# Kernel optimization log

Hardware: AMD Instinct MI355X
Metric: run time of the kernel (lower is better)

The kernel has to match this reference:

```python
import jax, jax.numpy as jnp
import numpy as np

HIDDEN = 64

def setup_inputs() -> dict:
    key = jax.random.key(0)
    ks = jax.random.split(key, 5)
    N, T, D, H = 4096, 128, 32, HIDDEN
    x = jax.random.normal(ks[0], (N, T, D), dtype=jnp.float32)
    adj_matrix = jax.random.uniform(ks[1], (N, N), dtype=jnp.float32) * (1.0 / N)
    weight_ih = jax.random.normal(ks[2], (D, 4 * H), dtype=jnp.float32) * (1.0 / np.sqrt(D))
    weight_hh = jax.random.normal(ks[3], (H, 4 * H), dtype=jnp.float32) * (1.0 / np.sqrt(H))
    bias = jnp.zeros((4 * H,), dtype=jnp.float32)
    weight_q = jax.random.normal(ks[4], (H, H), dtype=jnp.float32) * (1.0 / np.sqrt(H))
    bias_q = jnp.zeros((H,), dtype=jnp.float32)
    return {"x": x, "adj_matrix": adj_matrix, "weight_ih": weight_ih,
            "weight_hh": weight_hh, "bias": bias, "weight_q": weight_q,
            "bias_q": bias_q}

def reference(x, adj_matrix, weight_ih, weight_hh, bias, weight_q, bias_q):
    # x: [N, T, D]; adj_matrix: [N, N]. Dropout=0 -> identity (eval mode).
    N, T, D = x.shape
    H = weight_hh.shape[0]

    def step(carry, x_t):
        h, c = carry                                   # [N, H], [N, H]
        gates = x_t @ weight_ih + h @ weight_hh + bias  # [N, 4H]
        i_t = jax.nn.sigmoid(gates[:, :H])
        f_t = jax.nn.sigmoid(gates[:, H:2 * H])
        g_t = jnp.tanh(gates[:, 2 * H:3 * H])
        o_t = jax.nn.sigmoid(gates[:, 3 * H:])
        q_t = jnp.tanh(h @ weight_q + bias_q)           # [N, H]
        c_new = f_t * (c + adj_matrix @ q_t) + i_t * g_t
        h_new = o_t * jnp.tanh(c_new)
        return (h_new, c_new), h_new

    h0 = jnp.zeros((N, H), dtype=x.dtype)
    c0 = jnp.zeros((N, H), dtype=x.dtype)
    xs = jnp.swapaxes(x, 0, 1)                          # [T, N, D]
    _, hs = jax.lax.scan(step, (h0, c0), xs)            # hs: [T, N, H]
    return jnp.swapaxes(hs, 0, 1)                       # [N, T, H]
```

## Files before the change

### kernel.cpp

```cpp
#include <hip/hip_runtime.h>

typedef __attribute__((ext_vector_type(8))) short short8;
typedef __attribute__((ext_vector_type(4))) float f32x4;
typedef __attribute__((ext_vector_type(2))) float f32x2;
typedef __attribute__((ext_vector_type(2))) unsigned short us2;

#define N_NODES 4096
#define T_STEPS 128
#define H_DIM   64
#define NBLK    256
#define NTHR    512
#define ROWS    16

#define WS_FLAGS 0u
#define WS_WT    32768u
#define WS_WQT   81920u
#define WS_SYNC  90112u
#define WS_Q0    98304u
#define WS_Q1    360448u
#define WS_NEED  1146880u

#define ADJ_STRIDE_B 4112u
#define ADJ_BYTES  (16u * ADJ_STRIDE_B)
#define GATE_BYTES 16384u
#define S_BYTES    4224u
#define C_BYTES    4096u
#define H_BYTES    2304u
#define SMEM_TOT   (ADJ_BYTES + GATE_BYTES + S_BYTES + C_BYTES + H_BYTES)

__device__ __forceinline__ unsigned short f2bf(float f) {
    unsigned x = __float_as_uint(f);
    unsigned r = ((x >> 16) & 1u) + 0x7fffu;
    return (unsigned short)((x + r) >> 16);
}
__device__ __forceinline__ short8 cvt8_trunc_v(f32x4 a, f32x4 b) {
    union { unsigned u[4]; short8 s; } cv;
    cv.u[0] = __builtin_amdgcn_perm(__float_as_uint(a[1]), __float_as_uint(a[0]), 0x07060302u);
    cv.u[1] = __builtin_amdgcn_perm(__float_as_uint(a[3]), __float_as_uint(a[2]), 0x07060302u);
    cv.u[2] = __builtin_amdgcn_perm(__float_as_uint(b[1]), __float_as_uint(b[0]), 0x07060302u);
    cv.u[3] = __builtin_amdgcn_perm(__float_as_uint(b[3]), __float_as_uint(b[2]), 0x07060302u);
    return cv.s;
}
__device__ __forceinline__ float fast_sigmoid(float x) { return 1.f / (1.f + __expf(-x)); }
__device__ __forceinline__ float fast_tanh(float x)    { return 1.f - 2.f / (1.f + __expf(2.f * x)); }

__device__ __forceinline__ void grid_barrier(int* flags, int bid, int tid, int epoch) {
    __syncthreads();
    if (tid == 0) {
        __builtin_amdgcn_fence(__ATOMIC_RELEASE, "agent");
        __hip_atomic_store(&flags[bid * 32], epoch, __ATOMIC_RELAXED, __HIP_MEMORY_SCOPE_AGENT);
    }
    if (tid < NBLK) {
        int guard = 0;
        while (__hip_atomic_load(&flags[tid * 32], __ATOMIC_RELAXED, __HIP_MEMORY_SCOPE_AGENT) < epoch) {
            __builtin_amdgcn_s_sleep(32);
            if (++guard > (1 << 17)) break;
        }
    }
    __syncthreads();
    if (tid == 0) __builtin_amdgcn_fence(__ATOMIC_ACQUIRE, "agent");
    __syncthreads();
}

__device__ __forceinline__ void light_barrier(int* cnt, int bid, int tid, int arrivals) {
    asm volatile("s_waitcnt vmcnt(0)" ::: "memory");
    __syncthreads();
    if (tid == 0)
        __hip_atomic_fetch_add(&cnt[(bid & 7) * 32], 1, __ATOMIC_RELAXED, __HIP_MEMORY_SCOPE_AGENT);
    if (tid < 64) {
        const int target = arrivals * NBLK;
        int guard = 0;
        for (;;) {
            int v = (tid < 8)
                ? __hip_atomic_load(&cnt[tid * 32], __ATOMIC_RELAXED, __HIP_MEMORY_SCOPE_AGENT) : 0;
            v += __shfl_xor(v, 4);
            v += __shfl_xor(v, 2);
            v += __shfl_xor(v, 1);
            if (__builtin_amdgcn_readfirstlane(v) >= target) break;
            __builtin_amdgcn_s_sleep(8);
            if (++guard > (1 << 17)) break;
        }
    }
    __syncthreads();
}

#define MFMA16(a, b, c)  __builtin_amdgcn_mfma_f32_16x16x32_bf16((a), (b), (c), 0, 0, 0)
#define MFMAF8(a, b, c)  __builtin_amdgcn_mfma_f32_16x16x32_fp8_fp8((a), (b), (c), 0, 0, 0)

#define QLD(dst, ptr, off) \
    asm volatile("global_load_dwordx2 %0, %1, off offset:" #off " sc0 sc1" \
                 : "=v"(dst) : "v"(ptr))
#define ISSUE_G(dst, pp) do { \
    QLD((dst)[0], (pp), 0);    QLD((dst)[1], (pp), 512);  \
    QLD((dst)[2], (pp), 1024); QLD((dst)[3], (pp), 1536); \
    QLD((dst)[4], (pp), 2048); QLD((dst)[5], (pp), 2560); \
    QLD((dst)[6], (pp), 3072); QLD((dst)[7], (pp), 3584); \
} while (0)
#define WAITV(n) do { asm volatile("s_waitcnt vmcnt(" #n ")" ::: "memory"); \
                      __builtin_amdgcn_sched_barrier(0); } while (0)
#define MFMA_GRP(B) do { \
    acc[0] = MFMAF8(a0_, (B)[0], acc[0]); acc[1] = MFMAF8(a0_, (B)[1], acc[1]); \
    acc[2] = MFMAF8(a0_, (B)[2], acc[2]); acc[3] = MFMAF8(a0_, (B)[3], acc[3]); \
    acc[0] = MFMAF8(a1_, (B)[4], acc[0]); acc[1] = MFMAF8(a1_, (B)[5], acc[1]); \
    acc[2] = MFMAF8(a1_, (B)[6], acc[2]); acc[3] = MFMAF8(a1_, (B)[7], acc[3]); \
} while (0)

__global__ __launch_bounds__(NTHR, 1) void glstm_kernel(
    const float* __restrict__ x,
    const float* __restrict__ adj,
    const float* __restrict__ w_ih,
    const float* __restrict__ w_hh,
    const float* __restrict__ bias,
    const float* __restrict__ w_q,
    const float* __restrict__ bias_q,
    float* __restrict__ out,
    unsigned char* __restrict__ ws)
{
    const int tid  = threadIdx.x;
    const int bid  = blockIdx.x;
    const int wave = tid >> 6;
    const int lane = tid & 63;
    const int l15  = lane & 15;
    const int quad = lane >> 4;
    const int rowbase = bid * ROWS;

    int* flags = (int*)(ws + WS_FLAGS);
    int* cnt   = (int*)(ws + WS_SYNC);
    unsigned short* Wt  = (unsigned short*)(ws + WS_WT);
    unsigned short* Wqt = (unsigned short*)(ws + WS_WQT);
    unsigned char* qb0 = ws + WS_Q0;
    unsigned char* qb1 = ws + WS_Q1;

    extern __shared__ unsigned char smem[];
    unsigned char* adj_lds = smem;
    float* gate_lds = (float*)(smem + ADJ_BYTES);
    float* s_lds    = (float*)(smem + ADJ_BYTES + GATE_BYTES);
    float* c_lds    = (float*)(smem + ADJ_BYTES + GATE_BYTES + S_BYTES);
    unsigned short* h_lds = (unsigned short*)(smem + ADJ_BYTES + GATE_BYTES + S_BYTES + C_BYTES);

    if (tid < 96) {
        float v = (tid < 32) ? w_ih[tid * 256 + bid] : w_hh[(tid - 32) * 256 + bid];
        Wt[bid * 96 + tid] = f2bf(v);
    }
    if (bid < 64 && tid < 64) Wqt[bid * 64 + tid] = f2bf(w_q[tid * 64 + bid]);
    if (bid == 0 && tid < 8) cnt[tid * 32] = 0;
    for (int idx = tid; idx < ROWS * 64; idx += NTHR) {
        int r = idx >> 6, hh = idx & 63;
        float v = fast_tanh(bias_q[hh]);
        qb0[(size_t)(bid >> 1) * 2048 + (hh >> 4) * 512 + (hh & 15) * 32 + (bid & 1) * 16 + r]
            = (unsigned char)(__builtin_amdgcn_cvt_pk_fp8_f32(v, v, 0, false) & 0xFF);
    }
    for (int idx = tid; idx < ROWS * 64; idx += NTHR) {
        int r = idx >> 6, cc = idx & 63;
        c_lds[r * 64 + cc] = 0.f;
        s_lds[r * 66 + cc] = 0.f;
        h_lds[r * 72 + cc] = 0;
    }
    for (int idx = tid; idx < ROWS * (N_NODES / 2); idx += NTHR) {
        int r = idx >> 11, c2 = idx & (N_NODES / 2 - 1);
        f32x2 av = *(const f32x2*)(adj + (size_t)(rowbase + r) * N_NODES + c2 * 2);
        int pk = __builtin_amdgcn_cvt_pk_fp8_f32(av[0] * 4096.f, av[1] * 4096.f, 0, false);
        *(unsigned short*)(adj_lds + r * ADJ_STRIDE_B + c2 * 2) = (unsigned short)pk;
    }
    grid_barrier(flags, bid, tid, 1);

    const int g    = wave >> 1;
    const int half = wave & 1;
    const int nc0  = g * 64 + half * 32 + l15;
    short8 wA[2][3];
#pragma unroll
    for (int nt = 0; nt < 2; ++nt)
#pragma unroll
        for (int kk = 0; kk < 3; ++kk)
            wA[nt][kk] = *(const short8*)(Wt + (nc0 + nt * 16) * 96 + kk * 32 + quad * 8);
    const float bv0 = bias[nc0], bv1 = bias[nc0 + 16];
    const int hhq = (wave & 3) * 16 + l15;
    short8 wQ[2];
#pragma unroll
    for (int kk = 0; kk < 2; ++kk)
        wQ[kk] = *(const short8*)(Wqt + hhq * 64 + kk * 32 + quad * 8);
    const float bqv = bias_q[hhq];

    const float* xlane = x + (size_t)(rowbase + l15) * T_STEPS * 32 + quad * 8;
    const unsigned char* albase = adj_lds + l15 * ADJ_STRIDE_B + wave * 512 + quad * 8;
    const size_t qdoff = (size_t)(bid >> 1) * 2048 + (size_t)(wave & 3) * 512
                       + l15 * 32 + (bid & 1) * 16 + quad * 4;

    f32x4 xa = *(const f32x4*)(xlane);
    f32x4 xb = *(const f32x4*)(xlane + 4);

    auto phaseA = [&]() {
        f32x4 acc0 = {0.f, 0.f, 0.f, 0.f};
        f32x4 acc1 = {0.f, 0.f, 0.f, 0.f};
        short8 a0 = cvt8_trunc_v(xa, xb);
        acc0 = MFMA16(a0, wA[0][0], acc0);
        acc1 = MFMA16(a0, wA[1][0], acc1);
#pragma unroll
        for (int kk = 1; kk < 3; ++kk) {
            short8 a = *(const short8*)(h_lds + l15 * 72 + (kk - 1) * 32 + quad * 8);
            acc0 = MFMA16(a, wA[0][kk], acc0);
            acc1 = MFMA16(a, wA[1][kk], acc1);
        }
#pragma unroll
        for (int nt = 0; nt < 2; ++nt) {
            f32x4 acc = nt ? acc1 : acc0;
            float bv  = nt ? bv1 : bv0;
            int colg  = half * 32 + nt * 16 + l15;
#pragma unroll
            for (int r = 0; r < 4; ++r) {
                float v = acc[r] + bv;
                v = (g == 2) ? fast_tanh(v) : fast_sigmoid(v);
                gate_lds[(g * 16 + quad * 4 + r) * 64 + colg] = v;
            }
        }
    };

    phaseA();
    xa = *(const f32x4*)(xlane + 32);
    xb = *(const f32x4*)(xlane + 36);

    for (int t = 0; t < T_STEPS; ++t) {
        const unsigned char* qcur = (t & 1) ? qb1 : qb0;
        unsigned char*       qnxt = (t & 1) ? qb0 : qb1;

        {
            f32x4 acc[4];
#pragma unroll
            for (int nt = 0; nt < 4; ++nt) acc[nt] = (f32x4){0.f, 0.f, 0.f, 0.f};
            const unsigned char* qp = qcur + (size_t)(wave * 16) * 2048 + (l15 << 5) + (quad << 3);
            long qv2[2][8];
            long a0_ = *(const long*)(albase);
            long a1_ = *(const long*)(albase + 32);
            ISSUE_G(qv2[0], qp);
#pragma unroll
            for (int gg = 0; gg < 8; ++gg) {
                if (gg < 7) { const unsigned char* pg = qp + (gg + 1) * 4096; ISSUE_G(qv2[(gg + 1) & 1], pg); }
                long na0, na1;
                if (gg < 7) {
                    na0 = *(const long*)(albase + (gg + 1) * 64);
                    na1 = *(const long*)(albase + (gg + 1) * 64 + 32);
                    WAITV(8);
                } else {
                    WAITV(0);
                }
                MFMA_GRP(qv2[gg & 1]);
                if (gg < 7) { a0_ = na0; a1_ = na1; }
            }
#pragma unroll
            for (int nt = 0; nt < 4; ++nt)
#pragma unroll
                for (int r = 0; r < 4; ++r)
                    atomicAdd(&s_lds[(quad * 4 + r) * 66 + nt * 16 + l15],
                              acc[nt][r] * (1.0f / 4096.0f));
        }
        __syncthreads();

        {
            const int r  = tid >> 5;
            const int c0 = (tid & 31) * 2;
            float hn[2];
#pragma unroll
            for (int j = 0; j < 2; ++j) {
                int cc = c0 + j;
                float s = s_lds[r * 66 + cc];
                s_lds[r * 66 + cc] = 0.f;
                float iv = gate_lds[(0 * 16 + r) * 64 + cc];
                float fv = gate_lds[(1 * 16 + r) * 64 + cc];
                float gv = gate_lds[(2 * 16 + r) * 64 + cc];
                float ov = gate_lds[(3 * 16 + r) * 64 + cc];
                float cn = fv * (c_lds[r * 64 + cc] + s) + iv * gv;
                hn[j] = ov * fast_tanh(cn);
                c_lds[r * 64 + cc] = cn;
            }
            us2 hv; hv[0] = f2bf(hn[0]); hv[1] = f2bf(hn[1]);
            *(us2*)(h_lds + r * 72 + c0) = hv;
            *(f32x2*)(out + ((size_t)(rowbase + r) * T_STEPS + t) * H_DIM + c0) = (f32x2){hn[0], hn[1]};
        }
        __syncthreads();

        if (t < T_STEPS - 1) {
            if (wave < 4) {
                f32x4 acc = {0.f, 0.f, 0.f, 0.f};
#pragma unroll
                for (int kk = 0; kk < 2; ++kk) {
                    short8 a = *(const short8*)(h_lds + l15 * 72 + kk * 32 + quad * 8);
                    acc = MFMA16(a, wQ[kk], acc);
                }
                float q0 = fast_tanh(acc[0] + bqv), q1 = fast_tanh(acc[1] + bqv);
                float q2 = fast_tanh(acc[2] + bqv), q3 = fast_tanh(acc[3] + bqv);
                int pk = __builtin_amdgcn_cvt_pk_fp8_f32(q0, q1, 0, false);
                pk     = __builtin_amdgcn_cvt_pk_fp8_f32(q2, q3, pk, true);
                unsigned char* qdst = qnxt + qdoff;
                asm volatile("global_store_dword %0, %1, off sc0 sc1" :: "v"(qdst), "v"(pk) : "memory");
            }
            phaseA();
            if (t < T_STEPS - 2) {
                xa = *(const f32x4*)(xlane + (t + 2) * 32);
                xb = *(const f32x4*)(xlane + (t + 2) * 32 + 4);
            }
            light_barrier(cnt, bid, tid, t + 1);
        }
    }
}

extern "C" void kernel_launch(void* const* d_in, const int* in_sizes, int n_in,
                              void* d_out, int out_size, void* d_ws, size_t ws_size,
                              hipStream_t stream) {
    if (ws_size < WS_NEED) return;
    const float* x      = (const float*)d_in[0];
    const float* adj    = (const float*)d_in[1];
    const float* w_ih   = (const float*)d_in[2];
    const float* w_hh   = (const float*)d_in[3];
    const float* bias   = (const float*)d_in[4];
    const float* w_q    = (const float*)d_in[5];
    const float* bias_q = (const float*)d_in[6];
    float* o = (float*)d_out;
    unsigned char* w = (unsigned char*)d_ws;

    hipFuncSetAttribute((const void*)glstm_kernel,
                        hipFuncAttributeMaxDynamicSharedMemorySize, SMEM_TOT);
    glstm_kernel<<<NBLK, NTHR, SMEM_TOT, stream>>>(x, adj, w_ih, w_hh, bias, w_q, bias_q, o, w);
}
```

Before: 2.599 ms.

## Relayout fp8 q buffer for dwordx4 loads with triple-buffered prefetch

Changes the global fp8 q-state layout so that each lane's two K-halves for an MFMA tile sit contiguously. This lets the adjacency-times-q loop fetch them with four 16-byte loads per group instead of eight 8-byte loads. The pipeline goes from double to triple buffering, keeping two groups in flight ahead of compute. Both the writer side (qdoff, init) and the reader side are updated together. The aim is fewer load instructions and more latency hiding in the cross-block q fetch, at the cost of more registers.

```diff
diff --git a/kernel.cpp b/kernel.cpp
--- a/kernel.cpp
+++ b/kernel.cpp
@@ -4,6 +4,7 @@
 typedef __attribute__((ext_vector_type(4))) float f32x4;
 typedef __attribute__((ext_vector_type(2))) float f32x2;
 typedef __attribute__((ext_vector_type(2))) unsigned short us2;
+typedef __attribute__((ext_vector_type(2))) long lx2;
 
 #define N_NODES 4096
 #define T_STEPS 128
@@ -87,23 +88,15 @@
 #define MFMA16(a, b, c)  __builtin_amdgcn_mfma_f32_16x16x32_bf16((a), (b), (c), 0, 0, 0)
 #define MFMAF8(a, b, c)  __builtin_amdgcn_mfma_f32_16x16x32_fp8_fp8((a), (b), (c), 0, 0, 0)
 
-#define QLD(dst, ptr, off) \
-    asm volatile("global_load_dwordx2 %0, %1, off offset:" #off " sc0 sc1" \
+#define QLD4(dst, ptr, off) \
+    asm volatile("global_load_dwordx4 %0, %1, off offset:" #off " sc0 sc1" \
                  : "=v"(dst) : "v"(ptr))
-#define ISSUE_G(dst, pp) do { \
-    QLD((dst)[0], (pp), 0);    QLD((dst)[1], (pp), 512);  \
-    QLD((dst)[2], (pp), 1024); QLD((dst)[3], (pp), 1536); \
-    QLD((dst)[4], (pp), 2048); QLD((dst)[5], (pp), 2560); \
-    QLD((dst)[6], (pp), 3072); QLD((dst)[7], (pp), 3584); \
+#define ISSUE_ST(dst, pp) do { \
+    QLD4((dst)[0], (pp), 0);    QLD4((dst)[1], (pp), 1024); \
+    QLD4((dst)[2], (pp), 2048); QLD4((dst)[3], (pp), 3072); \
 } while (0)
 #define WAITV(n) do { asm volatile("s_waitcnt vmcnt(" #n ")" ::: "memory"); \
                       __builtin_amdgcn_sched_barrier(0); } while (0)
-#define MFMA_GRP(B) do { \
-    acc[0] = MFMAF8(a0_, (B)[0], acc[0]); acc[1] = MFMAF8(a0_, (B)[1], acc[1]); \
-    acc[2] = MFMAF8(a0_, (B)[2], acc[2]); acc[3] = MFMAF8(a0_, (B)[3], acc[3]); \
-    acc[0] = MFMAF8(a1_, (B)[4], acc[0]); acc[1] = MFMAF8(a1_, (B)[5], acc[1]); \
-    acc[2] = MFMAF8(a1_, (B)[6], acc[2]); acc[3] = MFMAF8(a1_, (B)[7], acc[3]); \
-} while (0)
 
 __global__ __launch_bounds__(NTHR, 1) void glstm_kernel(
     const float* __restrict__ x,
@@ -146,8 +139,10 @@
     if (bid == 0 && tid < 8) cnt[tid * 32] = 0;
     for (int idx = tid; idx < ROWS * 64; idx += NTHR) {
         int r = idx >> 6, hh = idx & 63;
+        int n = rowbase + r, no = n & 63;
         float v = fast_tanh(bias_q[hh]);
-        qb0[(size_t)(bid >> 1) * 2048 + (hh >> 4) * 512 + (hh & 15) * 32 + (bid & 1) * 16 + r]
+        qb0[(size_t)(n >> 6) * 4096 + (hh >> 4) * 1024 + (hh & 15) * 64
+            + ((no >> 3) & 3) * 16 + (no >> 5) * 8 + (no & 7)]
             = (unsigned char)(__builtin_amdgcn_cvt_pk_fp8_f32(v, v, 0, false) & 0xFF);
     }
     for (int idx = tid; idx < ROWS * 64; idx += NTHR) {
@@ -183,8 +178,9 @@
 
     const float* xlane = x + (size_t)(rowbase + l15) * T_STEPS * 32 + quad * 8;
     const unsigned char* albase = adj_lds + l15 * ADJ_STRIDE_B + wave * 512 + quad * 8;
-    const size_t qdoff = (size_t)(bid >> 1) * 2048 + (size_t)(wave & 3) * 512
-                       + l15 * 32 + (bid & 1) * 16 + quad * 4;
+    const int no0 = ((bid & 3) << 4) + (quad << 2);
+    const size_t qdoff = (size_t)(bid >> 2) * 4096 + (size_t)(wave & 3) * 1024
+                       + (size_t)l15 * 64 + ((no0 >> 3) & 3) * 16 + (no0 >> 5) * 8 + (no0 & 7);
 
     f32x4 xa = *(const f32x4*)(xlane);
     f32x4 xb = *(const f32x4*)(xlane + 4);
@@ -227,24 +223,26 @@
             f32x4 acc[4];
 #pragma unroll
             for (int nt = 0; nt < 4; ++nt) acc[nt] = (f32x4){0.f, 0.f, 0.f, 0.f};
-            const unsigned char* qp = qcur + (size_t)(wave * 16) * 2048 + (l15 << 5) + (quad << 3);
-            long qv2[2][8];
-            long a0_ = *(const long*)(albase);
-            long a1_ = *(const long*)(albase + 32);
-            ISSUE_G(qv2[0], qp);
+            const unsigned char* qp = qcur + ((size_t)wave << 15) + (l15 << 6) + (quad << 4);
+            lx2 buf[3][4];
+            ISSUE_ST(buf[0], qp);
+            ISSUE_ST(buf[1], qp + 4096);
 #pragma unroll
             for (int gg = 0; gg < 8; ++gg) {
-                if (gg < 7) { const unsigned char* pg = qp + (gg + 1) * 4096; ISSUE_G(qv2[(gg + 1) & 1], pg); }
-                long na0, na1;
-                if (gg < 7) {
-                    na0 = *(const long*)(albase + (gg + 1) * 64);
-                    na1 = *(const long*)(albase + (gg + 1) * 64 + 32);
-                    WAITV(8);
-                } else {
-                    WAITV(0);
-                }
-                MFMA_GRP(qv2[gg & 1]);
-                if (gg < 7) { a0_ = na0; a1_ = na1; }
+                if (gg < 6) { const unsigned char* pg = qp + (gg + 2) * 4096; ISSUE_ST(buf[(gg + 2) % 3], pg); }
+                long a0_ = *(const long*)(albase + gg * 64);
+                long a1_ = *(const long*)(albase + gg * 64 + 32);
+                if (gg < 6)       WAITV(8);
+                else if (gg == 6) WAITV(4);
+                else              WAITV(0);
+                acc[0] = MFMAF8(a0_, buf[gg % 3][0][0], acc[0]);
+                acc[1] = MFMAF8(a0_, buf[gg % 3][1][0], acc[1]);
+                acc[2] = MFMAF8(a0_, buf[gg % 3][2][0], acc[2]);
+                acc[3] = MFMAF8(a0_, buf[gg % 3][3][0], acc[3]);
+                acc[0] = MFMAF8(a1_, buf[gg % 3][0][1], acc[0]);
+                acc[1] = MFMAF8(a1_, buf[gg % 3][1][1], acc[1]);
+                acc[2] = MFMAF8(a1_, buf[gg % 3][2][1], acc[2]);
+                acc[3] = MFMAF8(a1_, buf[gg % 3][3][1], acc[3]);
             }
 #pragma unroll
             for (int nt = 0; nt < 4; ++nt)
```

Result: faster. 2.546 ms (-2.0%).
